# Optimization experiments

Measured on AMD Instinct MI355X. Metric: run time of the kernel, lower is better.

## Reference

```python
import jax, jax.numpy as jnp
import numpy as np

# Dims: batch, in-ch, out-ch, deform kernel, channels-per-offset-group, input H/W
B, CIN, COUT, K, CPG, H, W = 16, 64, 64, 3, 8, 130, 130
G = CIN // CPG                 # number of deformable offset groups = 8
HO, WO = H - 2, W - 2          # conv1 (3x3, VALID) output == deform-conv output (3x3, VALID)
DN = ('NCHW', 'OIHW', 'NCHW')


def _conv(x, w, b):
    y = jax.lax.conv_general_dilated(x, w, (1, 1), 'VALID', dimension_numbers=DN)
    return y + b[None, :, None, None]


def setup_inputs() -> dict:
    key = jax.random.key(0)
    k0, k1, k2, k3 = jax.random.split(key, 4)
    def wn(k, shape, fan_in, scale=1.0):
        return jax.random.normal(k, shape, jnp.float32) * (scale / np.sqrt(fan_in))
    return {
        'x':  jax.random.normal(k0, (B, CIN, H, W), jnp.float32),
        'w1': wn(k1, (CIN, CIN, 3, 3), CIN * 9),
        'b1': jnp.zeros((CIN,), jnp.float32),
        # small scale so predicted offsets stay in a realistic sub-pixel/pixel range
        'w2': wn(k2, (G * 2 * K * K, CIN, 1, 1), CIN, scale=0.1),
        'b2': jnp.zeros((G * 2 * K * K,), jnp.float32),
        'wd': wn(k3, (COUT, CIN, K, K), CIN * K * K),
    }


def _deform_conv(x, off, wd):
    # x: [B,CIN,H,W], off: [B,G*2*K*K,HO,WO], wd: [COUT,CIN,K,K]
    Bq, Cin, Hx, Wx = x.shape
    offr = off.reshape(Bq, G, K, K, 2, HO, WO)     # (dy, dx) per group/kernel-pos/pixel
    xg = x.reshape(Bq, G, CPG, Hx * Wx)            # grouped input, flat spatial
    hh = jnp.arange(HO, dtype=x.dtype)[:, None]
    ww = jnp.arange(WO, dtype=x.dtype)[None, :]
    out = jnp.zeros((Bq, COUT, HO, WO), x.dtype)

    def gather(yi, xi, valid):
        # yi/xi: clipped int coords [B,G,HO,WO]; valid: 0/1 mask (zero padding outside)
        idx = (yi * Wx + xi).reshape(Bq, G, 1, HO * WO)
        v = jnp.take_along_axis(xg, jnp.broadcast_to(idx, (Bq, G, CPG, HO * WO)), axis=-1)
        return v.reshape(Bq, G, CPG, HO, WO) * valid[:, :, None, :, :]

    for i in range(K):
        for j in range(K):
            py = offr[:, :, i, j, 0] + (hh + i)    # [B,G,HO,WO] sample row (float)
            px = offr[:, :, i, j, 1] + (ww + j)    # [B,G,HO,WO] sample col (float)
            y0 = jnp.floor(py); x0 = jnp.floor(px)
            ly = py - y0;       lx = px - x0
            y0i = y0.astype(jnp.int32); x0i = x0.astype(jnp.int32)
            y1i = y0i + 1;              x1i = x0i + 1
            inb = lambda yi, xi: ((yi >= 0) & (yi < Hx) & (xi >= 0) & (xi < Wx)).astype(x.dtype)
            yc0 = jnp.clip(y0i, 0, Hx - 1); yc1 = jnp.clip(y1i, 0, Hx - 1)
            xc0 = jnp.clip(x0i, 0, Wx - 1); xc1 = jnp.clip(x1i, 0, Wx - 1)
            v = (((1 - ly) * (1 - lx))[:, :, None] * gather(yc0, xc0, inb(y0i, x0i))
               + ((1 - ly) * lx)[:, :, None]       * gather(yc0, xc1, inb(y0i, x1i))
               + (ly * (1 - lx))[:, :, None]       * gather(yc1, xc0, inb(y1i, x0i))
               + (ly * lx)[:, :, None]             * gather(yc1, xc1, inb(y1i, x1i)))
            # accumulate this kernel tap: v [B,G,CPG,HO,WO] x wd[:,:,i,j] [COUT,G,CPG]
            out = out + jnp.einsum('bgchw,ogc->bohw', v, wd[:, :, i, j].reshape(COUT, G, CPG))
    return out


def reference(x, w1, b1, w2, b2, wd):
    off = _conv(_conv(x, w1, b1), w2, b2)          # [B, G*2*K*K, HO, WO]
    y = _deform_conv(x, off, wd)                   # [B, COUT, HO, WO]
    return (y, off)
```

## Files before the change

kernel.cpp:

```cpp
#include <hip/hip_runtime.h>

typedef unsigned short u16;
typedef unsigned int u32;
typedef __attribute__((ext_vector_type(8))) short bfrag;
typedef __attribute__((ext_vector_type(4))) float ffrag;

constexpr int B_ = 16, CIN = 64, COUT = 64, G = 8, CPG = 8;
constexpr int H = 130, W = 130, HO = 128, WO = 128;
constexpr int OFFC = 144;
constexpr int PLANE_IN = H * W;
constexpr int PLANE_OUT = HO * WO;

constexpr size_t WB1_BYTE = 36864 * 4;
constexpr size_t WB2_BYTE = WB1_BYTE + 36864 * 2;
constexpr size_t XT_BYTE  = 262144;
constexpr size_t XT_SIZE  = (size_t)B_ * PLANE_IN * 64 * 2;

__device__ __forceinline__ u16 f2bf(float f) {
    union { u32 u; float f; } t; t.f = f;
    return (u16)((t.u + 0x7FFFu + ((t.u >> 16) & 1u)) >> 16);
}
__device__ __forceinline__ float bf2f(short h) {
    union { u32 u; float f; } t; t.u = ((u32)(u16)h) << 16;
    return t.f;
}

__global__ void prep_weights(const float* __restrict__ w1,
                             const float* __restrict__ wd,
                             const float* __restrict__ w2,
                             float* __restrict__ wsf) {
    u16* wdB = (u16*)wsf;
    u16* wB1 = (u16*)((char*)wsf + WB1_BYTE);
    u16* wB2 = (u16*)((char*)wsf + WB2_BYTE);
    int idx = blockIdx.x * 256 + threadIdx.x;
    if (idx < 36864) {
        int co = idx / 576, r = idx % 576;
        int t = r >> 6, ci = r & 63;
        wdB[idx] = f2bf(wd[(co * 64 + ci) * 9 + t]);
    } else if (idx < 73728) {
        int j = idx - 36864;
        int co = j / 576, r = j % 576;
        int t = r >> 6, ci = r & 63;
        wB1[j] = f2bf(w1[(co * 64 + ci) * 9 + t]);
    } else if (idx < 82944) {
        int j = idx - 73728;
        wB2[j] = f2bf(w2[j]);
    }
}

__global__ __launch_bounds__(256) void x_to_nhwc(const float* __restrict__ x,
                                                 u16* __restrict__ xt) {
    int p = blockIdx.x * 256 + threadIdx.x;
    if (p >= B_ * PLANE_IN) return;
    int b = p / PLANE_IN, pp = p % PLANE_IN;
    const float* xb = x + (size_t)b * CIN * PLANE_IN + pp;
    u16* dst = xt + (size_t)p * 64;
    #pragma unroll
    for (int oct = 0; oct < 8; ++oct) {
        union { u16 h[8]; uint4 q; } pk;
        #pragma unroll
        for (int j = 0; j < 8; ++j)
            pk.h[j] = f2bf(xb[(size_t)(oct * 8 + j) * PLANE_IN]);
        *(uint4*)(dst + oct * 8) = pk.q;
    }
}

union ConvSmem {
    char xsb[324 * 128];
    char hsb[4][64 * 128];
};
__device__ __forceinline__ int swz128(int row, int bytecol) {
    return row * 128 + (bytecol ^ ((row & 7) << 4));
}

template<bool XT>
__global__ __launch_bounds__(256) void conv12(const float* __restrict__ x,
                                              const u16* __restrict__ xt,
                                              const float* __restrict__ b1,
                                              const float* __restrict__ b2,
                                              const float* __restrict__ wsf,
                                              float* __restrict__ off_out) {
    __shared__ ConvSmem sm;
    const u16* wB1 = (const u16*)((const char*)wsf + WB1_BYTE);
    const u16* wB2 = (const u16*)((const char*)wsf + WB2_BYTE);
    const int b = blockIdx.z;
    const int y0 = blockIdx.y * 16, x0 = blockIdx.x * 16;
    const int tid = threadIdx.x;
    const int wave = tid >> 6, lane = tid & 63;
    const int n16 = lane & 15, quad = lane >> 4;

    if constexpr (XT) {
        const u16* xtb = xt + (size_t)b * PLANE_IN * 64;
        for (int idx = tid; idx < 324 * 8; idx += 256) {
            int p = idx >> 3, oct = idx & 7;
            *(bfrag*)(sm.xsb + swz128(p, oct * 16)) =
                *(const bfrag*)&xtb[((size_t)(y0 + p / 18) * W + x0 + p % 18) * 64 + oct * 8];
        }
    } else {
        const float* xb = x + (size_t)b * CIN * PLANE_IN;
        for (int idx = tid; idx < 324 * 64; idx += 256) {
            int ci = idx / 324, p = idx % 324;
            float v = xb[(size_t)ci * PLANE_IN + (y0 + p / 18) * W + (x0 + p % 18)];
            *(u16*)(sm.xsb + swz128(p, ci * 2)) = f2bf(v);
        }
    }
    __syncthreads();

    ffrag acc[4][4];
    #pragma unroll
    for (int nt = 0; nt < 4; ++nt) {
        float bv = b1[nt * 16 + n16];
        #pragma unroll
        for (int mt = 0; mt < 4; ++mt) acc[mt][nt] = ffrag{bv, bv, bv, bv};
    }

    #pragma unroll
    for (int s = 0; s < 18; ++s) {
        const int tap = s >> 1, cib = (s & 1) * 32;
        const int ti = tap / 3, tj = tap % 3;
        bfrag a[4], bb[4];
        #pragma unroll
        for (int mt = 0; mt < 4; ++mt) {
            int p = (wave * 4 + mt + ti) * 18 + n16 + tj;
            a[mt] = *(const bfrag*)(sm.xsb + swz128(p, cib * 2 + quad * 16));
        }
        #pragma unroll
        for (int nt = 0; nt < 4; ++nt)
            bb[nt] = *(const bfrag*)&wB1[(nt * 16 + n16) * 576 + tap * 64 + cib + quad * 8];
        #pragma unroll
        for (int mt = 0; mt < 4; ++mt)
            #pragma unroll
            for (int nt = 0; nt < 4; ++nt)
                acc[mt][nt] = __builtin_amdgcn_mfma_f32_16x16x32_bf16(
                    a[mt], bb[nt], acc[mt][nt], 0, 0, 0);
    }

    __syncthreads();

    #pragma unroll
    for (int mt = 0; mt < 4; ++mt)
        #pragma unroll
        for (int nt = 0; nt < 4; ++nt)
            #pragma unroll
            for (int r = 0; r < 4; ++r)
                *(u16*)(sm.hsb[wave] + swz128(mt * 16 + quad * 4 + r, (nt * 16 + n16) * 2))
                    = f2bf(acc[mt][nt][r]);
    __syncthreads();

    bfrag a2[4][2];
    #pragma unroll
    for (int mt = 0; mt < 4; ++mt)
        #pragma unroll
        for (int s2 = 0; s2 < 2; ++s2)
            a2[mt][s2] = *(const bfrag*)(sm.hsb[wave]
                        + swz128(mt * 16 + n16, s2 * 64 + quad * 16));

    float* offb = off_out + (size_t)b * OFFC * PLANE_OUT;
    #pragma unroll 1
    for (int nt2 = 0; nt2 < 9; ++nt2) {
        bfrag b2f[2];
        #pragma unroll
        for (int s2 = 0; s2 < 2; ++s2)
            b2f[s2] = *(const bfrag*)&wB2[(nt2 * 16 + n16) * 64 + s2 * 32 + quad * 8];
        float bv = b2[nt2 * 16 + n16];
        #pragma unroll
        for (int mt = 0; mt < 4; ++mt) {
            ffrag acc2 = ffrag{bv, bv, bv, bv};
            acc2 = __builtin_amdgcn_mfma_f32_16x16x32_bf16(a2[mt][0], b2f[0], acc2, 0, 0, 0);
            acc2 = __builtin_amdgcn_mfma_f32_16x16x32_bf16(a2[mt][1], b2f[1], acc2, 0, 0, 0);
            float* dst = offb + (size_t)(nt2 * 16 + n16) * PLANE_OUT
                       + (y0 + wave * 4 + mt) * WO + x0 + quad * 4;
            *(ffrag*)dst = acc2;
        }
    }
}

__device__ __forceinline__ bfrag interp4(const bfrag* q, const float* w) {
    union { u16 h[8]; bfrag f; } pk;
    #pragma unroll
    for (int j = 0; j < 8; ++j) {
        float v = w[0] * bf2f(q[0][j]) + w[1] * bf2f(q[1][j])
                + w[2] * bf2f(q[2][j]) + w[3] * bf2f(q[3][j]);
        pk.h[j] = f2bf(v);
    }
    return pk.f;
}

template<bool XT>
__global__ __launch_bounds__(256, 2) void deform_k(const float* __restrict__ x,
                                                   const u16* __restrict__ xt,
                                                   const float* __restrict__ wsf,
                                                   const float* __restrict__ off_in,
                                                   float* __restrict__ y_out) {
    const u16* wdB = (const u16*)wsf;

    const int wg = blockIdx.x;
    const int swz = (wg & 7) * 256 + (wg >> 3);
    const int b = swz >> 7, sp = swz & 127;
    const int y0 = (sp >> 3) * 8, x0 = (sp & 7) * 16;

    const int tid = threadIdx.x;
    const int wave = tid >> 6, lane = tid & 63;
    const int n16 = lane & 15, quad = lane >> 4;
    const int wo = x0 + n16;

    const float* offbase = off_in + (size_t)b * OFFC * PLANE_OUT + x0 + n16;
    const u16* xtb = xt + (size_t)b * PLANE_IN * 64;
    const float* xb = x + (size_t)b * CIN * PLANE_IN;

    ffrag acc[2][4];
    #pragma unroll
    for (int mt = 0; mt < 2; ++mt)
        #pragma unroll
        for (int nt = 0; nt < 4; ++nt) acc[mt][nt] = ffrag{0.f, 0.f, 0.f, 0.f};

    float pdy[4], pdx[4];
    #pragma unroll
    for (int tk = 0; tk < 4; ++tk) {
        const int mt = tk >> 1, g = quad + (tk & 1) * 4;
        const float* ob = offbase + (y0 + wave * 2 + mt) * WO
                        + (size_t)(g * 9 * 2) * PLANE_OUT;
        pdy[tk] = ob[0];
        pdx[tk] = ob[PLANE_OUT];
    }

    #pragma unroll 1
    for (int t = 0; t < 9; ++t) {
        const int ki = t / 3, kj = t % 3;

        float dyv[4], dxv[4];
        #pragma unroll
        for (int tk = 0; tk < 4; ++tk) { dyv[tk] = pdy[tk]; dxv[tk] = pdx[tk]; }

        if (t < 8) {
            #pragma unroll
            for (int tk = 0; tk < 4; ++tk) {
                const int mt = tk >> 1, g = quad + (tk & 1) * 4;
                const float* ob = offbase + (y0 + wave * 2 + mt) * WO
                                + (size_t)((g * 9 + t + 1) * 2) * PLANE_OUT;
                pdy[tk] = ob[0];
                pdx[tk] = ob[PLANE_OUT];
            }
        }

        int idxq[4][4];
        float wq[4][4];
        #pragma unroll
        for (int tk = 0; tk < 4; ++tk) {
            const int mt = tk >> 1, g = quad + (tk & 1) * 4;
            const int ho = y0 + wave * 2 + mt;
            float py = dyv[tk] + (float)(ho + ki);
            float px = dxv[tk] + (float)(wo + kj);
            float y0f = floorf(py), x0f = floorf(px);
            float ly = py - y0f, lx = px - x0f;
            int yi0 = (int)y0f, xi0 = (int)x0f;
            int yi1 = yi0 + 1, xi1 = xi0 + 1;
            float vy0 = (yi0 >= 0 && yi0 < H) ? 1.f : 0.f;
            float vy1 = (yi1 >= 0 && yi1 < H) ? 1.f : 0.f;
            float vx0 = (xi0 >= 0 && xi0 < W) ? 1.f : 0.f;
            float vx1 = (xi1 >= 0 && xi1 < W) ? 1.f : 0.f;
            wq[tk][0] = (1.f - ly) * (1.f - lx) * vy0 * vx0;
            wq[tk][1] = (1.f - ly) * lx         * vy0 * vx1;
            wq[tk][2] = ly * (1.f - lx)         * vy1 * vx0;
            wq[tk][3] = ly * lx                 * vy1 * vx1;
            int yc0 = min(max(yi0, 0), H - 1), yc1 = min(max(yi1, 0), H - 1);
            int xc0 = min(max(xi0, 0), W - 1), xc1 = min(max(xi1, 0), W - 1);
            idxq[tk][0] = (yc0 * W + xc0) * 64 + g * 8;
            idxq[tk][1] = (yc0 * W + xc1) * 64 + g * 8;
            idxq[tk][2] = (yc1 * W + xc0) * 64 + g * 8;
            idxq[tk][3] = (yc1 * W + xc1) * 64 + g * 8;
        }

        bfrag frag[4];
        if constexpr (XT) {
            bfrag q0[4], q1[4], q2[4], q3[4];
            #pragma unroll
            for (int c = 0; c < 4; ++c) q0[c] = *(const bfrag*)&xtb[idxq[0][c]];
            #pragma unroll
            for (int c = 0; c < 4; ++c) q1[c] = *(const bfrag*)&xtb[idxq[1][c]];
            bfrag bw0[4], bw1[4];
            #pragma unroll
            for (int nt = 0; nt < 4; ++nt) {
                const u16* wp = &wdB[(size_t)(nt * 16 + n16) * 576 + t * 64 + quad * 8];
                bw0[nt] = *(const bfrag*)wp;
                bw1[nt] = *(const bfrag*)(wp + 32);
            }
            frag[0] = interp4(q0, wq[0]);
            #pragma unroll
            for (int c = 0; c < 4; ++c) q2[c] = *(const bfrag*)&xtb[idxq[2][c]];
            frag[1] = interp4(q1, wq[1]);
            #pragma unroll
            for (int c = 0; c < 4; ++c) q3[c] = *(const bfrag*)&xtb[idxq[3][c]];
            frag[2] = interp4(q2, wq[2]);
            frag[3] = interp4(q3, wq[3]);

            #pragma unroll
            for (int nt = 0; nt < 4; ++nt)
                #pragma unroll
                for (int mt = 0; mt < 2; ++mt) {
                    acc[mt][nt] = __builtin_amdgcn_mfma_f32_16x16x32_bf16(
                        frag[mt * 2 + 0], bw0[nt], acc[mt][nt], 0, 0, 0);
                    acc[mt][nt] = __builtin_amdgcn_mfma_f32_16x16x32_bf16(
                        frag[mt * 2 + 1], bw1[nt], acc[mt][nt], 0, 0, 0);
                }
        } else {
            #pragma unroll
            for (int tk = 0; tk < 4; ++tk) {
                const int g = quad + (tk & 1) * 4;
                const float* xg = xb + (size_t)g * CPG * PLANE_IN;
                union { u16 h[8]; bfrag f; } pk;
                #pragma unroll
                for (int cc = 0; cc < 8; ++cc) {
                    const float* xp = xg + cc * PLANE_IN;
                    int sh = (idxq[tk][0] - g * 8) / 64;
                    int s01 = (idxq[tk][1] - g * 8) / 64;
                    int s10 = (idxq[tk][2] - g * 8) / 64;
                    int s11 = (idxq[tk][3] - g * 8) / 64;
                    float v = wq[tk][0] * xp[sh] + wq[tk][1] * xp[s01]
                            + wq[tk][2] * xp[s10] + wq[tk][3] * xp[s11];
                    pk.h[cc] = f2bf(v);
                }
                frag[tk] = pk.f;
            }
            #pragma unroll
            for (int nt = 0; nt < 4; ++nt) {
                const u16* wp = &wdB[(size_t)(nt * 16 + n16) * 576 + t * 64 + quad * 8];
                bfrag b0 = *(const bfrag*)wp;
                bfrag b1 = *(const bfrag*)(wp + 32);
                #pragma unroll
                for (int mt = 0; mt < 2; ++mt) {
                    acc[mt][nt] = __builtin_amdgcn_mfma_f32_16x16x32_bf16(
                        frag[mt * 2 + 0], b0, acc[mt][nt], 0, 0, 0);
                    acc[mt][nt] = __builtin_amdgcn_mfma_f32_16x16x32_bf16(
                        frag[mt * 2 + 1], b1, acc[mt][nt], 0, 0, 0);
                }
            }
        }
    }

    float* yb = y_out + (size_t)b * COUT * PLANE_OUT;
    #pragma unroll
    for (int nt = 0; nt < 4; ++nt)
        #pragma unroll
        for (int mt = 0; mt < 2; ++mt) {
            float* dst = yb + (size_t)(nt * 16 + n16) * PLANE_OUT
                       + (y0 + wave * 2 + mt) * WO + x0 + quad * 4;
            *(ffrag*)dst = acc[mt][nt];
        }
}

extern "C" void kernel_launch(void* const* d_in, const int* in_sizes, int n_in,
                              void* d_out, int out_size, void* d_ws, size_t ws_size,
                              hipStream_t stream) {
    const float* x  = (const float*)d_in[0];
    const float* w1 = (const float*)d_in[1];
    const float* b1 = (const float*)d_in[2];
    const float* w2 = (const float*)d_in[3];
    const float* b2 = (const float*)d_in[4];
    const float* wd = (const float*)d_in[5];
    float* y_out = (float*)d_out;
    float* off_out = y_out + (size_t)B_ * COUT * PLANE_OUT;
    float* wsf = (float*)d_ws;
    u16* xt = (u16*)((char*)d_ws + XT_BYTE);
    const bool use_xt = ws_size >= XT_BYTE + XT_SIZE;

    prep_weights<<<324, 256, 0, stream>>>(w1, wd, w2, wsf);
    if (use_xt) {
        x_to_nhwc<<<(B_ * PLANE_IN + 255) / 256, 256, 0, stream>>>(x, xt);
        conv12<true><<<dim3(8, 8, B_), 256, 0, stream>>>(x, xt, b1, b2, wsf, off_out);
        deform_k<true><<<2048, 256, 0, stream>>>(x, xt, wsf, off_out, y_out);
    } else {
        conv12<false><<<dim3(8, 8, B_), 256, 0, stream>>>(x, xt, b1, b2, wsf, off_out);
        deform_k<false><<<2048, 256, 0, stream>>>(x, xt, wsf, off_out, y_out);
    }
}
```

Measured before the change: 530.2 us.

## Stage deform input tile with halo in LDS and gather bilinear taps from shared memory

```diff
diff --git a/kernel.cpp b/kernel.cpp
--- a/kernel.cpp
+++ b/kernel.cpp
@@ -186,18 +186,26 @@
     return pk.f;
 }
 
+constexpr int TR = 14, TC = 22, TILE_PX = TR * TC;
+
+__device__ __forceinline__ bfrag lds_px(const char* xls, int p, int g) {
+    return *(const bfrag*)(xls + p * 128 + ((g * 16) ^ ((p & 7) << 4)));
+}
+
 template<bool XT>
-__global__ __launch_bounds__(256, 2) void deform_k(const float* __restrict__ x,
+__global__ __launch_bounds__(256, 4) void deform_k(const float* __restrict__ x,
                                                    const u16* __restrict__ xt,
                                                    const float* __restrict__ wsf,
                                                    const float* __restrict__ off_in,
                                                    float* __restrict__ y_out) {
+    __shared__ char xls[TILE_PX * 128];
     const u16* wdB = (const u16*)wsf;
 
     const int wg = blockIdx.x;
     const int swz = (wg & 7) * 256 + (wg >> 3);
     const int b = swz >> 7, sp = swz & 127;
     const int y0 = (sp >> 3) * 8, x0 = (sp & 7) * 16;
+    const int ylo = y0 - 2, xlo = x0 - 2;
 
     const int tid = threadIdx.x;
     const int wave = tid >> 6, lane = tid & 63;
@@ -207,6 +215,18 @@
     const float* offbase = off_in + (size_t)b * OFFC * PLANE_OUT + x0 + n16;
     const u16* xtb = xt + (size_t)b * PLANE_IN * 64;
     const float* xb = x + (size_t)b * CIN * PLANE_IN;
+
+    if constexpr (XT) {
+        for (int idx = tid; idx < TILE_PX * 8; idx += 256) {
+            int oct = idx & 7, pix = idx >> 3;
+            int ty = pix / TC, tx = pix % TC;
+            int iy = min(max(ylo + ty, 0), H - 1);
+            int ix = min(max(xlo + tx, 0), W - 1);
+            *(bfrag*)(xls + pix * 128 + ((oct * 16) ^ ((pix & 7) << 4)))
+                = *(const bfrag*)&xtb[((size_t)(iy * W + ix)) * 64 + oct * 8];
+        }
+        __syncthreads();
+    }
 
     ffrag acc[2][4];
     #pragma unroll
@@ -243,8 +263,15 @@
             }
         }
 
-        int idxq[4][4];
-        float wq[4][4];
+        bfrag bw0[4], bw1[4];
+        #pragma unroll
+        for (int nt = 0; nt < 4; ++nt) {
+            const u16* wp = &wdB[(size_t)(nt * 16 + n16) * 576 + t * 64 + quad * 8];
+            bw0[nt] = *(const bfrag*)wp;
+            bw1[nt] = *(const bfrag*)(wp + 32);
+        }
+
+        bfrag frag[4];
         #pragma unroll
         for (int tk = 0; tk < 4; ++tk) {
             const int mt = tk >> 1, g = quad + (tk & 1) * 4;
@@ -259,83 +286,64 @@
             float vy1 = (yi1 >= 0 && yi1 < H) ? 1.f : 0.f;
             float vx0 = (xi0 >= 0 && xi0 < W) ? 1.f : 0.f;
             float vx1 = (xi1 >= 0 && xi1 < W) ? 1.f : 0.f;
-            wq[tk][0] = (1.f - ly) * (1.f - lx) * vy0 * vx0;
-            wq[tk][1] = (1.f - ly) * lx         * vy0 * vx1;
-            wq[tk][2] = ly * (1.f - lx)         * vy1 * vx0;
-            wq[tk][3] = ly * lx                 * vy1 * vx1;
+            float wq[4];
+            wq[0] = (1.f - ly) * (1.f - lx) * vy0 * vx0;
+            wq[1] = (1.f - ly) * lx         * vy0 * vx1;
+            wq[2] = ly * (1.f - lx)         * vy1 * vx0;
+            wq[3] = ly * lx                 * vy1 * vx1;
             int yc0 = min(max(yi0, 0), H - 1), yc1 = min(max(yi1, 0), H - 1);
             int xc0 = min(max(xi0, 0), W - 1), xc1 = min(max(xi1, 0), W - 1);
-            idxq[tk][0] = (yc0 * W + xc0) * 64 + g * 8;
-            idxq[tk][1] = (yc0 * W + xc1) * 64 + g * 8;
-            idxq[tk][2] = (yc1 * W + xc0) * 64 + g * 8;
-            idxq[tk][3] = (yc1 * W + xc1) * 64 + g * 8;
-        }
-
-        bfrag frag[4];
-        if constexpr (XT) {
-            bfrag q0[4], q1[4], q2[4], q3[4];
-            #pragma unroll
-            for (int c = 0; c < 4; ++c) q0[c] = *(const bfrag*)&xtb[idxq[0][c]];
-            #pragma unroll
-            for (int c = 0; c < 4; ++c) q1[c] = *(const bfrag*)&xtb[idxq[1][c]];
-            bfrag bw0[4], bw1[4];
-            #pragma unroll
-            for (int nt = 0; nt < 4; ++nt) {
-                const u16* wp = &wdB[(size_t)(nt * 16 + n16) * 576 + t * 64 + quad * 8];
-                bw0[nt] = *(const bfrag*)wp;
-                bw1[nt] = *(const bfrag*)(wp + 32);
-            }
-            frag[0] = interp4(q0, wq[0]);
-            #pragma unroll
-            for (int c = 0; c < 4; ++c) q2[c] = *(const bfrag*)&xtb[idxq[2][c]];
-            frag[1] = interp4(q1, wq[1]);
-            #pragma unroll
-            for (int c = 0; c < 4; ++c) q3[c] = *(const bfrag*)&xtb[idxq[3][c]];
-            frag[2] = interp4(q2, wq[2]);
-            frag[3] = interp4(q3, wq[3]);
-
-            #pragma unroll
-            for (int nt = 0; nt < 4; ++nt)
-                #pragma unroll
-                for (int mt = 0; mt < 2; ++mt) {
-                    acc[mt][nt] = __builtin_amdgcn_mfma_f32_16x16x32_bf16(
-                        frag[mt * 2 + 0], bw0[nt], acc[mt][nt], 0, 0, 0);
-                    acc[mt][nt] = __builtin_amdgcn_mfma_f32_16x16x32_bf16(
-                        frag[mt * 2 + 1], bw1[nt], acc[mt][nt], 0, 0, 0);
+
+            if constexpr (XT) {
+                int ry0 = yc0 - ylo, ry1 = yc1 - ylo;
+                int rx0 = xc0 - xlo, rx1 = xc1 - xlo;
+                bool intile = ((u32)ry0 < TR) & ((u32)ry1 < TR)
+                            & ((u32)rx0 < TC) & ((u32)rx1 < TC);
+                int p00 = ry0 * TC + rx0, p01 = ry0 * TC + rx1;
+                int p10 = ry1 * TC + rx0, p11 = ry1 * TC + rx1;
+                p00 = min(max(p00, 0), TILE_PX - 1);
+                p01 = min(max(p01, 0), TILE_PX - 1);
+                p10 = min(max(p10, 0), TILE_PX - 1);
+                p11 = min(max(p11, 0), TILE_PX - 1);
+                bfrag q[4];
+                q[0] = lds_px(xls, p00, g);
+                q[1] = lds_px(xls, p01, g);
+                q[2] = lds_px(xls, p10, g);
+                q[3] = lds_px(xls, p11, g);
+                frag[tk] = interp4(q, wq);
+                if (!intile) {
+                    bfrag qg[4];
+                    qg[0] = *(const bfrag*)&xtb[(size_t)(yc0 * W + xc0) * 64 + g * 8];
+                    qg[1] = *(const bfrag*)&xtb[(size_t)(yc0 * W + xc1) * 64 + g * 8];
+                    qg[2] = *(const bfrag*)&xtb[(size_t)(yc1 * W + xc0) * 64 + g * 8];
+                    qg[3] = *(const bfrag*)&xtb[(size_t)(yc1 * W + xc1) * 64 + g * 8];
+                    frag[tk] = interp4(qg, wq);
                 }
-        } else {
-            #pragma unroll
-            for (int tk = 0; tk < 4; ++tk) {
-                const int g = quad + (tk & 1) * 4;
+            } else {
+                int i00 = yc0 * W + xc0, i01 = yc0 * W + xc1;
+                int i10 = yc1 * W + xc0, i11 = yc1 * W + xc1;
                 const float* xg = xb + (size_t)g * CPG * PLANE_IN;
                 union { u16 h[8]; bfrag f; } pk;
                 #pragma unroll
                 for (int cc = 0; cc < 8; ++cc) {
                     const float* xp = xg + cc * PLANE_IN;
-                    int sh = (idxq[tk][0] - g * 8) / 64;
-                    int s01 = (idxq[tk][1] - g * 8) / 64;
-                    int s10 = (idxq[tk][2] - g * 8) / 64;
-                    int s11 = (idxq[tk][3] - g * 8) / 64;
-                    float v = wq[tk][0] * xp[sh] + wq[tk][1] * xp[s01]
-                            + wq[tk][2] * xp[s10] + wq[tk][3] * xp[s11];
+                    float v = wq[0] * xp[i00] + wq[1] * xp[i01]
+                            + wq[2] * xp[i10] + wq[3] * xp[i11];
                     pk.h[cc] = f2bf(v);
                 }
                 frag[tk] = pk.f;
             }
+        }
+
+        #pragma unroll
+        for (int nt = 0; nt < 4; ++nt)
             #pragma unroll
-            for (int nt = 0; nt < 4; ++nt) {
-                const u16* wp = &wdB[(size_t)(nt * 16 + n16) * 576 + t * 64 + quad * 8];
-                bfrag b0 = *(const bfrag*)wp;
-                bfrag b1 = *(const bfrag*)(wp + 32);
-                #pragma unroll
-                for (int mt = 0; mt < 2; ++mt) {
-                    acc[mt][nt] = __builtin_amdgcn_mfma_f32_16x16x32_bf16(
-                        frag[mt * 2 + 0], b0, acc[mt][nt], 0, 0, 0);
-                    acc[mt][nt] = __builtin_amdgcn_mfma_f32_16x16x32_bf16(
-                        frag[mt * 2 + 1], b1, acc[mt][nt], 0, 0, 0);
-                }
+            for (int mt = 0; mt < 2; ++mt) {
+                acc[mt][nt] = __builtin_amdgcn_mfma_f32_16x16x32_bf16(
+                    frag[mt * 2 + 0], bw0[nt], acc[mt][nt], 0, 0, 0);
+                acc[mt][nt] = __builtin_amdgcn_mfma_f32_16x16x32_bf16(
+                    frag[mt * 2 + 1], bw1[nt], acc[mt][nt], 0, 0, 0);
             }
-        }
     }
 
     float* yb = y_out + (size_t)b * COUT * PLANE_OUT;
```

Result: slower. 548.4 us (+3.4%).
